# Kernel optimization log

Hardware: AMD Instinct MI355X
Metric: run time of the kernel (lower is better)

Reference implementation:

```python
import jax, jax.numpy as jnp
import numpy as np

N_NODES = 100000
DIM = 128
N_REL = 8
N_EDGES = 640000
LAMDA = 1  # indexes into [x, z1, z2]


def setup_inputs() -> dict:
    key = jax.random.key(0)
    ks = jax.random.split(key, 6)
    x = jax.random.normal(ks[0], (N_NODES, DIM), dtype=jnp.float32)
    edge_index = jax.random.randint(ks[1], (2, N_EDGES), 0, N_NODES, dtype=jnp.int32)
    edge_type = jax.random.randint(ks[2], (N_EDGES,), 0, N_REL, dtype=jnp.int32)
    edge_weight = jax.random.uniform(ks[3], (N_EDGES,), dtype=jnp.float32)
    # xavier_uniform for [R, in, out] weight stacks (fan_in=DIM, fan_out=DIM)
    limit = float(np.sqrt(6.0 / (DIM + DIM)))
    W1 = jax.random.uniform(ks[4], (N_REL, DIM, DIM), jnp.float32, -limit, limit)
    W2 = jax.random.uniform(ks[5], (N_REL, DIM, DIM), jnp.float32, -limit, limit)
    b1 = jnp.zeros((DIM,), jnp.float32)
    b2 = jnp.zeros((DIM,), jnp.float32)
    return {"x": x, "edge_index": edge_index, "edge_type": edge_type,
            "edge_weight": edge_weight, "W1": W1, "b1": b1, "W2": W2, "b2": b2}


def _ecge_conv(x, W, b, row, col, edge_type, coef, n_nodes):
    # Faithful to: msg_e = norm_e * w_e * (x[row_e] @ W[type_e]); out = scatter_add(msg, col) + b
    # Efficient form: transform every node by every relation once (N,R,D), then gather per edge.
    xW = jnp.einsum('ni,rio->nro', x, W)          # [N, R, D]
    msg = xW[row, edge_type] * coef[:, None]       # [E, D]
    out = jax.ops.segment_sum(msg, col, num_segments=n_nodes)
    return out + b


def reference(x, edge_index, edge_type, edge_weight, W1, b1, W2, b2):
    n_nodes = x.shape[0]
    row, col = edge_index[0], edge_index[1]
    # symmetric degree normalization based on destination (col) degree
    deg = jax.ops.segment_sum(jnp.ones_like(edge_weight), col, num_segments=n_nodes)
    deg_inv_sqrt = jnp.where(deg > 0, deg ** -0.5, 0.0)
    norm = deg_inv_sqrt[row] * deg_inv_sqrt[col]
    coef = norm * edge_weight

    z1 = jax.nn.relu(_ecge_conv(x, W1, b1, row, col, edge_type, coef, n_nodes))
    # F.dropout with training=False (eval mode) is identity
    z2 = _ecge_conv(z1, W2, b2, row, col, edge_type, coef, n_nodes)

    z_star = (x + z1 + z2) / 4.0
    temp = [x, z1, z2]
    z_sharp = temp[LAMDA]
    for i in range(LAMDA + 1, 3):
        z_sharp = z_sharp + temp[i]
    z_sharp = z_sharp / (4.0 - LAMDA)
    return (z_star, z_sharp)
```

## Files before the change

### kernel.cpp

```cpp
#include <hip/hip_runtime.h>
#include <hip/hip_bf16.h>
#include <cstdint>
#include <cstddef>

#define DIM  128
#define NREL 8
#define SCB  4096
#define CPB  16

typedef __attribute__((ext_vector_type(8))) short short8;
typedef __attribute__((ext_vector_type(4))) float f32x4;

static inline int cdiv(int a, int b){ return (a + b - 1) / b; }

__device__ inline uint32_t packrn(float lo, float hi){
    __hip_bfloat162 h = __float22bfloat162_rn(make_float2(lo, hi));
    union { __hip_bfloat162 h; uint32_t u; } v; v.h = h; return v.u;
}
__device__ inline float bf2f(uint32_t lo16){
    union { uint32_t u; float f; } v; v.u = lo16 << 16; return v.f;
}
__device__ inline float asf(int u){
    union { int i; float f; } v; v.i = u; return v.f;
}

__global__ __launch_bounds__(256) void k_prep(const float* __restrict__ x, unsigned short* __restrict__ xb, int n4,
                                              const int* __restrict__ col, const int* __restrict__ et, int E,
                                              int* __restrict__ cnt8, int nb4, int eb,
                                              const float* __restrict__ W1, const float* __restrict__ W2,
                                              unsigned short* __restrict__ wpk){
    int blk = blockIdx.x;
    if (blk < nb4){
        int i = blk * 256 + threadIdx.x;
        if (i >= n4) return;
        f32x4 v = __builtin_nontemporal_load((const f32x4*)x + i);
        uint2 o; o.x = packrn(v.x, v.y); o.y = packrn(v.z, v.w);
        *(uint2*)(xb + (size_t)i * 4) = o;
    } else if (blk < nb4 + eb){
        int e = (blk - nb4) * 256 + threadIdx.x;
        if (e < E) atomicAdd(&cnt8[col[e] * NREL + et[e]], 1);
    } else {
        int b = (blk - nb4 - eb) * 4 + (threadIdx.x >> 6);
        int lane = threadIdx.x & 63;
        int ks = b & 3, nt = (b >> 2) & 7, slot = b >> 5;
        const float* Wsrc = (slot < 8) ? (W1 + (size_t)slot * DIM * DIM)
                                       : (W2 + (size_t)(slot - 8) * DIM * DIM);
        int k0 = ks * 32 + (lane >> 4) * 8;
        int n  = nt * 16 + (lane & 15);
        uint4 ow;
        ow.x = packrn(Wsrc[(size_t)(k0 + 0) * DIM + n], Wsrc[(size_t)(k0 + 1) * DIM + n]);
        ow.y = packrn(Wsrc[(size_t)(k0 + 2) * DIM + n], Wsrc[(size_t)(k0 + 3) * DIM + n]);
        ow.z = packrn(Wsrc[(size_t)(k0 + 4) * DIM + n], Wsrc[(size_t)(k0 + 5) * DIM + n]);
        ow.w = packrn(Wsrc[(size_t)(k0 + 6) * DIM + n], Wsrc[(size_t)(k0 + 7) * DIM + n]);
        *(uint4*)(wpk + ((size_t)b * 64 + lane) * 8) = ow;
    }
}

__global__ __launch_bounds__(256) void k_scan1(const int* __restrict__ cnt, int M, int* __restrict__ bsum){
    int t = threadIdx.x;
    int base = blockIdx.x * SCB + t * 16;
    int s = 0;
    #pragma unroll
    for (int k = 0; k < 16; ++k){
        int i = base + k;
        if (i < M) s += cnt[i];
    }
    #pragma unroll
    for (int o = 1; o < 64; o <<= 1) s += __shfl_xor(s, o);
    __shared__ int wsum[4];
    if ((t & 63) == 0) wsum[t >> 6] = s;
    __syncthreads();
    if (t == 0) bsum[blockIdx.x] = wsum[0] + wsum[1] + wsum[2] + wsum[3];
}

__global__ __launch_bounds__(256) void k_scan3(const int* __restrict__ cnt, int M,
                                               const int* __restrict__ bsum, int NBS,
                                               int* __restrict__ startArr, int* __restrict__ pos,
                                               float* __restrict__ deginv){
    int t = threadIdx.x;
    int base = blockIdx.x * SCB + t * 16;
    int vals[16];
    int s = 0;
    #pragma unroll
    for (int k = 0; k < 16; ++k){
        int i = base + k;
        vals[k] = (i < M) ? cnt[i] : 0;
        s += vals[k];
    }

    {
        int d0 = 0, d1 = 0;
        #pragma unroll
        for (int k = 0; k < 8; ++k){ d0 += vals[k]; d1 += vals[8 + k]; }
        int c0i = base >> 3;
        if (base < M)     deginv[c0i]     = d0 > 0 ? rsqrtf((float)d0) : 0.f;
        if (base + 8 < M) deginv[c0i + 1] = d1 > 0 ? rsqrtf((float)d1) : 0.f;
    }

    int lane = t & 63, w = t >> 6;

    int bp = 0, tp = 0;
    for (int i = lane; i < NBS; i += 64){
        int bv = bsum[i];
        if (i < (int)blockIdx.x) bp += bv;
        tp += bv;
    }
    #pragma unroll
    for (int o = 1; o < 64; o <<= 1){ bp += __shfl_xor(bp, o); tp += __shfl_xor(tp, o); }

    int v = s;
    #pragma unroll
    for (int o = 1; o < 64; o <<= 1){
        int u = __shfl_up(v, o);
        if (lane >= o) v += u;
    }
    __shared__ int wsum[4];
    if (lane == 63) wsum[w] = v;
    __syncthreads();
    int excl = v - s + bp;
    for (int i = 0; i < w; ++i) excl += wsum[i];
    #pragma unroll
    for (int k = 0; k < 16; ++k){
        int i = base + k;
        if (i < M){ startArr[i] = excl; pos[i] = excl; excl += vals[k]; }
    }
    if (blockIdx.x == (unsigned)(gridDim.x - 1) && t == 0) startArr[M] = tp;
}

__global__ __launch_bounds__(256) void k_place(const int* __restrict__ row, const int* __restrict__ col,
                                               const int* __restrict__ et, const float* __restrict__ ew,
                                               const float* __restrict__ deginv,
                                               int E, int* __restrict__ pos8, int2* __restrict__ pkm){
    int e = blockIdx.x * 256 + threadIdx.x;
    if (e >= E) return;
    int r = row[e], c = col[e], t = et[e];
    float cf = deginv[r] * deginv[c] * ew[e];
    int p = atomicAdd(&pos8[(c << 3) + t], 1);
    union { float f; int i; } cv; cv.f = cf;
    pkm[p] = make_int2(((c & (CPB - 1)) << 28) | (t << 25) | r, cv.i);
}

template<int MODE>
__global__ __launch_bounds__(512, 8) void k_fused(const unsigned short* __restrict__ xbin,
                                                  const unsigned short* __restrict__ wpk,
                                                  const int* __restrict__ cs8,
                                                  const int2* __restrict__ pkm,
                                                  const float* __restrict__ bias,
                                                  unsigned short* __restrict__ zb,
                                                  const unsigned short* __restrict__ xb2,
                                                  const unsigned short* __restrict__ z1b2,
                                                  float* __restrict__ outS,
                                                  float* __restrict__ outH,
                                                  int N, int wslot){
    __shared__ unsigned short s[CPB * 1024];
    int tid = threadIdx.x;
    int wid = tid >> 6, lane = tid & 63;
    int c0 = blockIdx.x * CPB;

    uint4 z4 = {0u, 0u, 0u, 0u};
    #pragma unroll
    for (int k = 0; k < 4; ++k) ((uint4*)s)[tid + 512 * k] = z4;
    __syncthreads();

#define FLUSH() *(uint32_t*)((char*)s + flushByte) = packrn(a0, a1)
#define PROC(mx, cf, u) do{                                                       \
        int fk_ = (int)(((unsigned)(mx)) >> 25);                                  \
        if (fk_ != fkPrev){                                                       \
            if (fkPrev >= 0) FLUSH();                                             \
            fkPrev = fk_;                                                         \
            flushByte = (fk_ << 8) + ((lane << 2) ^ ((fk_ << 1) & 0x70));         \
            a0 = 0.f; a1 = 0.f;                                                   \
        }                                                                         \
        a0 = fmaf(cf, bf2f((u) & 0xFFFFu), a0);                                   \
        a1 = fmaf(cf, bf2f((u) >> 16),     a1); }while(0)
#define XROW(mx) ((const uint32_t*)xbin)[((size_t)(((mx) & 0x1FFFF) << 6)) + lane]

    {
        int c = c0 + wid * 2;
        if (c < N){
            int cHi = c + 2; if (cHi > N) cHi = N;
            int e  = __builtin_amdgcn_readfirstlane(cs8[c * NREL]);
            int eE = __builtin_amdgcn_readfirstlane(cs8[cHi * NREL]);
            int fkPrev = -1;
            int flushByte = 0;
            float a0 = 0.f, a1 = 0.f;
            const int* __restrict__ mp = (const int*)pkm;
            while (e < eE){
                int n = eE - e; if (n > 16) n = 16;
                int mxs[16]; float cfs[16]; uint32_t u[16];
                int mprev = 0;
                #pragma unroll
                for (int k = 0; k < 16; ++k){
                    int live = k < n;
                    int raw  = mp[2 * (e + k)];
                    float rc = asf(mp[2 * (e + k) + 1]);
                    int mx = (k == 0) ? raw : (live ? raw : mprev);
                    mxs[k] = mx; mprev = mx;
                    cfs[k] = live ? rc : 0.f;
                }
                #pragma unroll
                for (int k = 0; k < 16; ++k) u[k] = XROW(mxs[k]);
                __builtin_amdgcn_sched_barrier(0);
                #pragma unroll
                for (int k = 0; k < 16; ++k) PROC(mxs[k], cfs[k], u[k]);
                e += n;
            }
            if (fkPrev >= 0) FLUSH();
        }
    }
#undef PROC
#undef FLUSH
#undef XROW
    __syncthreads();

    int nt = wid;
    f32x4 acc = (f32x4){0,0,0,0};

    int al = lane & 15, ak2 = (lane >> 4) * 16;
    int swz = (al & 7) << 4;
    const char* rowA = (const char*)s + al * 2048;

    const short8* bbase = (const short8*)wpk + (size_t)wslot * 2048 + lane;

    __builtin_amdgcn_s_setprio(1);
    #pragma unroll 4
    for (int ksg = 0; ksg < 32; ++ksg){
        int off = (ksg * 64 + ak2) ^ swz;
        short8 A = *(const short8*)(rowA + off);
        int t = ksg >> 2, ksl = ksg & 3;
        short8 B = (bbase + (size_t)t * 2048)[(nt * 4 + ksl) * 64];
        acc = __builtin_amdgcn_mfma_f32_16x16x32_bf16(A, B, acc, 0, 0, 0);
    }
    __builtin_amdgcn_s_setprio(0);
    __syncthreads();

    float* ot = (float*)s;
    int crb = (lane >> 4) * 4, dcl = lane & 15;
    {
        int d = nt * 16 + dcl;
        float bv = bias[d];
        #pragma unroll
        for (int r = 0; r < 4; ++r){
            int mrow = crb + r;
            float v = acc[r] + bv;
            if (MODE == 0) v = fmaxf(v, 0.f);
            ot[mrow * DIM + d] = v;
        }
    }
    __syncthreads();

    if (MODE == 0){
        if (tid < 256){
            int rowi = tid >> 4, seg = tid & 15;
            int c = c0 + rowi;
            if (c < N){
                const float* src = ot + rowi * DIM + seg * 8;
                uint4 vv;
                vv.x = packrn(src[0], src[1]);
                vv.y = packrn(src[2], src[3]);
                vv.z = packrn(src[4], src[5]);
                vv.w = packrn(src[6], src[7]);
                *(uint4*)(zb + ((size_t)c << 7) + seg * 8) = vv;
            }
        }
    } else {
        int rowi = tid >> 5, q = tid & 31;
        int c = c0 + rowi;
        if (c < N){
            int d0 = q * 4;
            size_t o = ((size_t)c << 7) + d0;
            ushort4 xv4 = *(const ushort4*)(xb2 + o);
            ushort4 zv4 = *(const ushort4*)(z1b2 + o);
            const float* src = ot + rowi * DIM + d0;
            f32x4 S, H;
            {
                float xv = bf2f(xv4.x), z1 = bf2f(zv4.x), v = src[0];
                S.x = (xv + z1 + v) * 0.25f; H.x = (z1 + v) * (1.0f / 3.0f);
            }
            {
                float xv = bf2f(xv4.y), z1 = bf2f(zv4.y), v = src[1];
                S.y = (xv + z1 + v) * 0.25f; H.y = (z1 + v) * (1.0f / 3.0f);
            }
            {
                float xv = bf2f(xv4.z), z1 = bf2f(zv4.z), v = src[2];
                S.z = (xv + z1 + v) * 0.25f; H.z = (z1 + v) * (1.0f / 3.0f);
            }
            {
                float xv = bf2f(xv4.w), z1 = bf2f(zv4.w), v = src[3];
                S.w = (xv + z1 + v) * 0.25f; H.w = (z1 + v) * (1.0f / 3.0f);
            }
            __builtin_nontemporal_store(S, (f32x4*)(outS + o));
            __builtin_nontemporal_store(H, (f32x4*)(outH + o));
        }
    }
}

extern "C" void kernel_launch(void* const* d_in, const int* in_sizes, int n_in,
                              void* d_out, int out_size, void* d_ws, size_t ws_size,
                              hipStream_t stream) {
    const float* x  = (const float*)d_in[0];
    const int*   ei = (const int*)d_in[1];
    const int*   et = (const int*)d_in[2];
    const float* ew = (const float*)d_in[3];
    const float* W1 = (const float*)d_in[4];
    const float* b1 = (const float*)d_in[5];
    const float* W2 = (const float*)d_in[6];
    const float* b2 = (const float*)d_in[7];

    int E = in_sizes[2];
    int N = in_sizes[0] / DIM;
    const int* row = ei;
    const int* col = ei + E;

    float* out = (float*)d_out;
    int ND  = N * DIM;
    int ND4 = ND / 4;
    float* zS = out;
    float* zH = out + ND;

    int M8   = N * NREL;
    int NBS8 = cdiv(M8, SCB);

    char* wsb = (char*)d_ws;
    size_t off = 0;
    auto take = [&](size_t bytes) -> char* {
        char* p = wsb + off;
        off = (off + bytes + 255) & ~(size_t)255;
        return p;
    };
    int*            cnt8     = (int*)           take((size_t)M8 * 4);
    int*            start8   = (int*)           take(((size_t)M8 + 1) * 4);
    int*            pos8     = (int*)           take((size_t)M8 * 4);
    int*            bsum     = (int*)           take(((size_t)NBS8 + 1) * 4);
    float*          deginv   = (float*)         take((size_t)N * 4);
    int2*           pkm      = (int2*)          take(((size_t)E + 16) * 8);
    unsigned short* wpk      = (unsigned short*)take((size_t)16 * 2048 * 8 * 2);
    unsigned short* xb       = (unsigned short*)take((size_t)ND * 2);
    unsigned short* z1b      = (unsigned short*)take((size_t)ND * 2);
    (void)n_in; (void)out_size; (void)ws_size;

    (void)hipMemsetAsync(cnt8, 0, (size_t)M8 * 4, stream);

    int eb  = cdiv(E, 256);
    int nb4 = cdiv(ND4, 256);
    k_prep  <<<nb4 + eb + 128, 256, 0, stream>>>(x, xb, ND4, col, et, E, cnt8, nb4, eb, W1, W2, wpk);
    k_scan1 <<<NBS8, 256, 0, stream>>>(cnt8, M8, bsum);
    k_scan3 <<<NBS8, 256, 0, stream>>>(cnt8, M8, bsum, NBS8, start8, pos8, deginv);
    k_place <<<eb, 256, 0, stream>>>(row, col, et, ew, deginv, E, pos8, pkm);

    int fb = cdiv(N, CPB);
    k_fused<0><<<fb, 512, 0, stream>>>(xb, wpk, start8, pkm, b1, z1b, nullptr, nullptr, nullptr, nullptr, N, 0);
    k_fused<1><<<fb, 512, 0, stream>>>(z1b, wpk, start8, pkm, b2, nullptr, xb, z1b, zS, zH, N, 8);
}
```

Measured before the change: 252.5 us.

## Make fused gather-GEMM kernel persistent and prefetch the next tile's gathers during MFMA

The fused aggregate-then-transform kernel becomes persistent, launched with at most 1024 blocks that stride over node tiles. Before each tile's MFMA loop, the first 16 edges of the next tile have their metadata and x rows loaded into registers, so those gather latencies can overlap the matrix multiply and epilogue. LDS is re-zeroed inside the loop instead of once per block. This trades launch and tail cost for higher register pressure (48 extra prefetch registers per thread), a hard grid cap that may reduce occupancy, and two extra barriers per tile.

```diff
diff --git a/kernel.cpp b/kernel.cpp
--- a/kernel.cpp
+++ b/kernel.cpp
@@ -151,15 +151,16 @@
                                                   const unsigned short* __restrict__ z1b2,
                                                   float* __restrict__ outS,
                                                   float* __restrict__ outH,
-                                                  int N, int wslot){
+                                                  int N, int NT, int wslot){
     __shared__ unsigned short s[CPB * 1024];
     int tid = threadIdx.x;
     int wid = tid >> 6, lane = tid & 63;
-    int c0 = blockIdx.x * CPB;
-
-    uint4 z4 = {0u, 0u, 0u, 0u};
-    #pragma unroll
-    for (int k = 0; k < 4; ++k) ((uint4*)s)[tid + 512 * k] = z4;
+    const int stride = gridDim.x;
+    const int* __restrict__ mp = (const int*)pkm;
+
+    uint4 z4v = {0u, 0u, 0u, 0u};
+    #pragma unroll
+    for (int k = 0; k < 4; ++k) ((uint4*)s)[tid + 512 * k] = z4v;
     __syncthreads();
 
 #define FLUSH() *(uint32_t*)((char*)s + flushByte) = packrn(a0, a1)
@@ -175,16 +176,17 @@
         a1 = fmaf(cf, bf2f((u) >> 16),     a1); }while(0)
 #define XROW(mx) ((const uint32_t*)xbin)[((size_t)(((mx) & 0x1FFFF) << 6)) + lane]
 
+    int t0 = blockIdx.x;
+    if (t0 >= NT) return;
+
     {
-        int c = c0 + wid * 2;
+        int c = t0 * CPB + wid * 2;
         if (c < N){
             int cHi = c + 2; if (cHi > N) cHi = N;
             int e  = __builtin_amdgcn_readfirstlane(cs8[c * NREL]);
             int eE = __builtin_amdgcn_readfirstlane(cs8[cHi * NREL]);
-            int fkPrev = -1;
-            int flushByte = 0;
+            int fkPrev = -1, flushByte = 0;
             float a0 = 0.f, a1 = 0.f;
-            const int* __restrict__ mp = (const int*)pkm;
             while (e < eE){
                 int n = eE - e; if (n > 16) n = 16;
                 int mxs[16]; float cfs[16]; uint32_t u[16];
@@ -208,91 +210,161 @@
             if (fkPrev >= 0) FLUSH();
         }
     }
+    __syncthreads();
+
+    int al = lane & 15, ak2 = (lane >> 4) * 16;
+    int swz = (al & 7) << 4;
+    const char* rowA = (const char*)s + al * 2048;
+    const short8* bbase = (const short8*)wpk + (size_t)wslot * 2048 + lane;
+    float* ot = (float*)s;
+    int nt = wid, crb = (lane >> 4) * 4, dcl = lane & 15;
+
+    for (int t = t0; t < NT; t += stride){
+        int nxt = t + stride;
+        bool hasN = nxt < NT;
+
+        int n0 = 0, ge = 0, geE = 0;
+        int gmx[16]; float gcf[16]; uint32_t gu[16];
+        if (hasN){
+            int c = nxt * CPB + wid * 2;
+            if (c < N){
+                int cHi = c + 2; if (cHi > N) cHi = N;
+                ge  = __builtin_amdgcn_readfirstlane(cs8[c * NREL]);
+                geE = __builtin_amdgcn_readfirstlane(cs8[cHi * NREL]);
+                n0 = geE - ge; if (n0 > 16) n0 = 16;
+                if (n0 > 0){
+                    int mprev = 0;
+                    #pragma unroll
+                    for (int k = 0; k < 16; ++k){
+                        int live = k < n0;
+                        int raw  = mp[2 * (ge + k)];
+                        float rc = asf(mp[2 * (ge + k) + 1]);
+                        int mx = (k == 0) ? raw : (live ? raw : mprev);
+                        gmx[k] = mx; mprev = mx;
+                        gcf[k] = live ? rc : 0.f;
+                    }
+                    #pragma unroll
+                    for (int k = 0; k < 16; ++k) gu[k] = XROW(gmx[k]);
+                    ge += n0;
+                }
+            }
+        }
+
+        f32x4 acc = (f32x4){0,0,0,0};
+        __builtin_amdgcn_s_setprio(1);
+        #pragma unroll 4
+        for (int ksg = 0; ksg < 32; ++ksg){
+            int off = (ksg * 64 + ak2) ^ swz;
+            short8 A = *(const short8*)(rowA + off);
+            int tt = ksg >> 2, ksl = ksg & 3;
+            short8 B = (bbase + (size_t)tt * 2048)[(nt * 4 + ksl) * 64];
+            acc = __builtin_amdgcn_mfma_f32_16x16x32_bf16(A, B, acc, 0, 0, 0);
+        }
+        __builtin_amdgcn_s_setprio(0);
+        __syncthreads();
+
+        {
+            int d = nt * 16 + dcl;
+            float bv = bias[d];
+            #pragma unroll
+            for (int r = 0; r < 4; ++r){
+                float v = acc[r] + bv;
+                if (MODE == 0) v = fmaxf(v, 0.f);
+                ot[(crb + r) * DIM + d] = v;
+            }
+            uint4* zp = (uint4*)((char*)s + 8192);
+            #pragma unroll
+            for (int k = 0; k < 3; ++k) zp[tid + 512 * k] = z4v;
+        }
+        __syncthreads();
+
+        {
+            f32x4 zf = (f32x4){0,0,0,0};
+            if (MODE == 0){
+                if (tid < 256){
+                    int rowi = tid >> 4, seg = tid & 15;
+                    int c = t * CPB + rowi;
+                    float* src = ot + rowi * DIM + seg * 8;
+                    if (c < N){
+                        uint4 vv;
+                        vv.x = packrn(src[0], src[1]);
+                        vv.y = packrn(src[2], src[3]);
+                        vv.z = packrn(src[4], src[5]);
+                        vv.w = packrn(src[6], src[7]);
+                        *(uint4*)(zb + ((size_t)c << 7) + seg * 8) = vv;
+                    }
+                    *(f32x4*)src = zf;
+                    *(f32x4*)(src + 4) = zf;
+                }
+            } else {
+                int rowi = tid >> 5, q = tid & 31;
+                int c = t * CPB + rowi;
+                int d0 = q * 4;
+                float* src = ot + rowi * DIM + d0;
+                if (c < N){
+                    size_t o = ((size_t)c << 7) + d0;
+                    ushort4 xv4 = *(const ushort4*)(xb2 + o);
+                    ushort4 zv4 = *(const ushort4*)(z1b2 + o);
+                    f32x4 S, H;
+                    {
+                        float xv = bf2f(xv4.x), z1 = bf2f(zv4.x), v = src[0];
+                        S.x = (xv + z1 + v) * 0.25f; H.x = (z1 + v) * (1.0f / 3.0f);
+                    }
+                    {
+                        float xv = bf2f(xv4.y), z1 = bf2f(zv4.y), v = src[1];
+                        S.y = (xv + z1 + v) * 0.25f; H.y = (z1 + v) * (1.0f / 3.0f);
+                    }
+                    {
+                        float xv = bf2f(xv4.z), z1 = bf2f(zv4.z), v = src[2];
+                        S.z = (xv + z1 + v) * 0.25f; H.z = (z1 + v) * (1.0f / 3.0f);
+                    }
+                    {
+                        float xv = bf2f(xv4.w), z1 = bf2f(zv4.w), v = src[3];
+                        S.w = (xv + z1 + v) * 0.25f; H.w = (z1 + v) * (1.0f / 3.0f);
+                    }
+                    __builtin_nontemporal_store(S, (f32x4*)(outS + o));
+                    __builtin_nontemporal_store(H, (f32x4*)(outH + o));
+                }
+                *(f32x4*)src = zf;
+            }
+        }
+        __syncthreads();
+
+        if (hasN){
+            int c = nxt * CPB + wid * 2;
+            if (c < N && n0 > 0){
+                int fkPrev = -1, flushByte = 0;
+                float a0 = 0.f, a1 = 0.f;
+                #pragma unroll
+                for (int k = 0; k < 16; ++k) PROC(gmx[k], gcf[k], gu[k]);
+                while (ge < geE){
+                    int n = geE - ge; if (n > 16) n = 16;
+                    int mxs[16]; float cfs[16]; uint32_t u[16];
+                    int mprev = 0;
+                    #pragma unroll
+                    for (int k = 0; k < 16; ++k){
+                        int live = k < n;
+                        int raw  = mp[2 * (ge + k)];
+                        float rc = asf(mp[2 * (ge + k) + 1]);
+                        int mx = (k == 0) ? raw : (live ? raw : mprev);
+                        mxs[k] = mx; mprev = mx;
+                        cfs[k] = live ? rc : 0.f;
+                    }
+                    #pragma unroll
+                    for (int k = 0; k < 16; ++k) u[k] = XROW(mxs[k]);
+                    __builtin_amdgcn_sched_barrier(0);
+                    #pragma unroll
+                    for (int k = 0; k < 16; ++k) PROC(mxs[k], cfs[k], u[k]);
+                    ge += n;
+                }
+                if (fkPrev >= 0) FLUSH();
+            }
+        }
+        __syncthreads();
+    }
 #undef PROC
 #undef FLUSH
 #undef XROW
-    __syncthreads();
-
-    int nt = wid;
-    f32x4 acc = (f32x4){0,0,0,0};
-
-    int al = lane & 15, ak2 = (lane >> 4) * 16;
-    int swz = (al & 7) << 4;
-    const char* rowA = (const char*)s + al * 2048;
-
-    const short8* bbase = (const short8*)wpk + (size_t)wslot * 2048 + lane;
-
-    __builtin_amdgcn_s_setprio(1);
-    #pragma unroll 4
-    for (int ksg = 0; ksg < 32; ++ksg){
-        int off = (ksg * 64 + ak2) ^ swz;
-        short8 A = *(const short8*)(rowA + off);
-        int t = ksg >> 2, ksl = ksg & 3;
-        short8 B = (bbase + (size_t)t * 2048)[(nt * 4 + ksl) * 64];
-        acc = __builtin_amdgcn_mfma_f32_16x16x32_bf16(A, B, acc, 0, 0, 0);
-    }
-    __builtin_amdgcn_s_setprio(0);
-    __syncthreads();
-
-    float* ot = (float*)s;
-    int crb = (lane >> 4) * 4, dcl = lane & 15;
-    {
-        int d = nt * 16 + dcl;
-        float bv = bias[d];
-        #pragma unroll
-        for (int r = 0; r < 4; ++r){
-            int mrow = crb + r;
-            float v = acc[r] + bv;
-            if (MODE == 0) v = fmaxf(v, 0.f);
-            ot[mrow * DIM + d] = v;
-        }
-    }
-    __syncthreads();
-
-    if (MODE == 0){
-        if (tid < 256){
-            int rowi = tid >> 4, seg = tid & 15;
-            int c = c0 + rowi;
-            if (c < N){
-                const float* src = ot + rowi * DIM + seg * 8;
-                uint4 vv;
-                vv.x = packrn(src[0], src[1]);
-                vv.y = packrn(src[2], src[3]);
-                vv.z = packrn(src[4], src[5]);
-                vv.w = packrn(src[6], src[7]);
-                *(uint4*)(zb + ((size_t)c << 7) + seg * 8) = vv;
-            }
-        }
-    } else {
-        int rowi = tid >> 5, q = tid & 31;
-        int c = c0 + rowi;
-        if (c < N){
-            int d0 = q * 4;
-            size_t o = ((size_t)c << 7) + d0;
-            ushort4 xv4 = *(const ushort4*)(xb2 + o);
-            ushort4 zv4 = *(const ushort4*)(z1b2 + o);
-            const float* src = ot + rowi * DIM + d0;
-            f32x4 S, H;
-            {
-                float xv = bf2f(xv4.x), z1 = bf2f(zv4.x), v = src[0];
-                S.x = (xv + z1 + v) * 0.25f; H.x = (z1 + v) * (1.0f / 3.0f);
-            }
-            {
-                float xv = bf2f(xv4.y), z1 = bf2f(zv4.y), v = src[1];
-                S.y = (xv + z1 + v) * 0.25f; H.y = (z1 + v) * (1.0f / 3.0f);
-            }
-            {
-                float xv = bf2f(xv4.z), z1 = bf2f(zv4.z), v = src[2];
-                S.z = (xv + z1 + v) * 0.25f; H.z = (z1 + v) * (1.0f / 3.0f);
-            }
-            {
-                float xv = bf2f(xv4.w), z1 = bf2f(zv4.w), v = src[3];
-                S.w = (xv + z1 + v) * 0.25f; H.w = (z1 + v) * (1.0f / 3.0f);
-            }
-            __builtin_nontemporal_store(S, (f32x4*)(outS + o));
-            __builtin_nontemporal_store(H, (f32x4*)(outH + o));
-        }
-    }
 }
 
 extern "C" void kernel_launch(void* const* d_in, const int* in_sizes, int n_in,
@@ -349,6 +421,8 @@
     k_place <<<eb, 256, 0, stream>>>(row, col, et, ew, deginv, E, pos8, pkm);
 
     int fb = cdiv(N, CPB);
-    k_fused<0><<<fb, 512, 0, stream>>>(xb, wpk, start8, pkm, b1, z1b, nullptr, nullptr, nullptr, nullptr, N, 0);
-    k_fused<1><<<fb, 512, 0, stream>>>(z1b, wpk, start8, pkm, b2, nullptr, xb, z1b, zS, zH, N, 8);
-}
+    int pg = 1024;
+    if (pg > fb) pg = fb;
+    k_fused<0><<<pg, 512, 0, stream>>>(xb, wpk, start8, pkm, b1, z1b, nullptr, nullptr, nullptr, nullptr, N, fb, 0);
+    k_fused<1><<<pg, 512, 0, stream>>>(z1b, wpk, start8, pkm, b2, nullptr, xb, z1b, zS, zH, N, fb, 8);
+}
```

Result: slower. 650.0 us (+157.4%).

## Balance edge aggregation across warps by edge chunks instead of node pairs

Applied to the files above, without the earlier changes.

Edge aggregation inside a block is no longer split as two destination nodes per warp. Each warp now takes fixed 16-edge chunks of the block's edge range, interleaved across the 8 warps. Each chunk boundary is moved to the next change of (col, relation) key so that every shared-memory slot is written by exactly one warp. This targets load imbalance from skewed node degrees, at the cost of scanning keys at chunk boundaries. Very long runs of one key can still fall to a single warp.

```diff
diff --git a/kernel.cpp b/kernel.cpp
--- a/kernel.cpp
+++ b/kernel.cpp
@@ -176,24 +176,35 @@
 #define XROW(mx) ((const uint32_t*)xbin)[((size_t)(((mx) & 0x1FFFF) << 6)) + lane]
 
     {
-        int c = c0 + wid * 2;
-        if (c < N){
-            int cHi = c + 2; if (cHi > N) cHi = N;
-            int e  = __builtin_amdgcn_readfirstlane(cs8[c * NREL]);
-            int eE = __builtin_amdgcn_readfirstlane(cs8[cHi * NREL]);
-            int fkPrev = -1;
-            int flushByte = 0;
-            float a0 = 0.f, a1 = 0.f;
-            const int* __restrict__ mp = (const int*)pkm;
-            while (e < eE){
-                int n = eE - e; if (n > 16) n = 16;
+        int cHi = c0 + CPB; if (cHi > N) cHi = N;
+        int e0 = __builtin_amdgcn_readfirstlane(cs8[c0 * NREL]);
+        int eT = __builtin_amdgcn_readfirstlane(cs8[cHi * NREL]);
+        int fkPrev = -1, flushByte = 0;
+        float a0 = 0.f, a1 = 0.f;
+        const int* __restrict__ mp = (const int*)pkm;
+
+        for (int b0 = e0 + wid * 16; b0 < eT; b0 += 8 * 16){
+            int bE = b0 + 16; if (bE > eT) bE = eT;
+            int sb = b0;
+            if (b0 > e0){
+                unsigned kp = ((unsigned)mp[2 * (b0 - 1)]) >> 25;
+                while (sb < bE && (((unsigned)mp[2 * sb]) >> 25) == kp) ++sb;
+            }
+            if (sb >= bE) continue;
+            int tE = bE;
+            {
+                unsigned kl = ((unsigned)mp[2 * (bE - 1)]) >> 25;
+                while (tE < eT && (((unsigned)mp[2 * tE]) >> 25) == kl) ++tE;
+            }
+            while (sb < tE){
+                int n = tE - sb; if (n > 16) n = 16;
                 int mxs[16]; float cfs[16]; uint32_t u[16];
                 int mprev = 0;
                 #pragma unroll
                 for (int k = 0; k < 16; ++k){
                     int live = k < n;
-                    int raw  = mp[2 * (e + k)];
-                    float rc = asf(mp[2 * (e + k) + 1]);
+                    int raw  = mp[2 * (sb + k)];
+                    float rc = asf(mp[2 * (sb + k) + 1]);
                     int mx = (k == 0) ? raw : (live ? raw : mprev);
                     mxs[k] = mx; mprev = mx;
                     cfs[k] = live ? rc : 0.f;
@@ -203,10 +214,10 @@
                 __builtin_amdgcn_sched_barrier(0);
                 #pragma unroll
                 for (int k = 0; k < 16; ++k) PROC(mxs[k], cfs[k], u[k]);
-                e += n;
-            }
-            if (fkPrev >= 0) FLUSH();
+                sb += n;
+            }
         }
+        if (fkPrev >= 0) FLUSH();
     }
 #undef PROC
 #undef FLUSH
```

Measured after the change: 283.9 us. 1.12x slower.

## Raise fused aggregate-transform tile from 16 to 20 destination nodes per block

Applied to the files above, without the earlier changes.

Grows the per-block destination-node tile from 16 to 20, so the bf16 relation-weight matrix streamed into the MFMA loop is reused over more rows. The edge packing is changed to hold a non-power-of-two local column index. Each wave now aggregates a variable 2-3 node range, and the GEMM issues a second MFMA per k-step for rows 16-19, with the remaining rows clamped. This adds LDS use (40KB per block) and wasted MFMA work on 12 padded rows, which may lower occupancy and unbalance the waves.

```diff
diff --git a/kernel.cpp b/kernel.cpp
--- a/kernel.cpp
+++ b/kernel.cpp
@@ -6,7 +6,7 @@
 #define DIM  128
 #define NREL 8
 #define SCB  4096
-#define CPB  16
+#define CPB  20
 
 typedef __attribute__((ext_vector_type(8))) short short8;
 typedef __attribute__((ext_vector_type(4))) float f32x4;
@@ -136,8 +136,9 @@
     int r = row[e], c = col[e], t = et[e];
     float cf = deginv[r] * deginv[c] * ew[e];
     int p = atomicAdd(&pos8[(c << 3) + t], 1);
+    int cl = c - (c / CPB) * CPB;
     union { float f; int i; } cv; cv.f = cf;
-    pkm[p] = make_int2(((c & (CPB - 1)) << 28) | (t << 25) | r, cv.i);
+    pkm[p] = make_int2((cl << 20) | (t << 17) | r, cv.i);
 }
 
 template<int MODE>
@@ -159,12 +160,12 @@
 
     uint4 z4 = {0u, 0u, 0u, 0u};
     #pragma unroll
-    for (int k = 0; k < 4; ++k) ((uint4*)s)[tid + 512 * k] = z4;
+    for (int k = 0; k < 5; ++k) ((uint4*)s)[tid + 512 * k] = z4;
     __syncthreads();
 
 #define FLUSH() *(uint32_t*)((char*)s + flushByte) = packrn(a0, a1)
 #define PROC(mx, cf, u) do{                                                       \
-        int fk_ = (int)(((unsigned)(mx)) >> 25);                                  \
+        int fk_ = (int)(((unsigned)(mx)) >> 17);                                  \
         if (fk_ != fkPrev){                                                       \
             if (fkPrev >= 0) FLUSH();                                             \
             fkPrev = fk_;                                                         \
@@ -176,13 +177,14 @@
 #define XROW(mx) ((const uint32_t*)xbin)[((size_t)(((mx) & 0x1FFFF) << 6)) + lane]
 
     {
-        int c = c0 + wid * 2;
-        if (c < N){
-            int cHi = c + 2; if (cHi > N) cHi = N;
-            int e  = __builtin_amdgcn_readfirstlane(cs8[c * NREL]);
+        int cLo = c0 + ((wid * CPB) >> 3);
+        int cHi = c0 + (((wid + 1) * CPB) >> 3);
+        if (cLo > N) cLo = N;
+        if (cHi > N) cHi = N;
+        if (cLo < cHi){
+            int e  = __builtin_amdgcn_readfirstlane(cs8[cLo * NREL]);
             int eE = __builtin_amdgcn_readfirstlane(cs8[cHi * NREL]);
-            int fkPrev = -1;
-            int flushByte = 0;
+            int fkPrev = -1, flushByte = 0;
             float a0 = 0.f, a1 = 0.f;
             const int* __restrict__ mp = (const int*)pkm;
             while (e < eE){
@@ -214,11 +216,13 @@
     __syncthreads();
 
     int nt = wid;
-    f32x4 acc = (f32x4){0,0,0,0};
+    f32x4 acc0 = (f32x4){0,0,0,0}, acc1 = (f32x4){0,0,0,0};
 
     int al = lane & 15, ak2 = (lane >> 4) * 16;
     int swz = (al & 7) << 4;
-    const char* rowA = (const char*)s + al * 2048;
+    const char* rowA0 = (const char*)s + al * 2048;
+    int r1c = 16 + al; if (r1c > CPB - 1) r1c = CPB - 1;
+    const char* rowA1 = (const char*)s + r1c * 2048;
 
     const short8* bbase = (const short8*)wpk + (size_t)wslot * 2048 + lane;
 
@@ -226,10 +230,12 @@
     #pragma unroll 4
     for (int ksg = 0; ksg < 32; ++ksg){
         int off = (ksg * 64 + ak2) ^ swz;
-        short8 A = *(const short8*)(rowA + off);
+        short8 A0 = *(const short8*)(rowA0 + off);
+        short8 A1 = *(const short8*)(rowA1 + off);
         int t = ksg >> 2, ksl = ksg & 3;
         short8 B = (bbase + (size_t)t * 2048)[(nt * 4 + ksl) * 64];
-        acc = __builtin_amdgcn_mfma_f32_16x16x32_bf16(A, B, acc, 0, 0, 0);
+        acc0 = __builtin_amdgcn_mfma_f32_16x16x32_bf16(A0, B, acc0, 0, 0, 0);
+        acc1 = __builtin_amdgcn_mfma_f32_16x16x32_bf16(A1, B, acc1, 0, 0, 0);
     }
     __builtin_amdgcn_s_setprio(0);
     __syncthreads();
@@ -241,16 +247,22 @@
         float bv = bias[d];
         #pragma unroll
         for (int r = 0; r < 4; ++r){
-            int mrow = crb + r;
-            float v = acc[r] + bv;
-            if (MODE == 0) v = fmaxf(v, 0.f);
-            ot[mrow * DIM + d] = v;
+            int row0 = crb + r;
+            float v0 = acc0[r] + bv;
+            if (MODE == 0) v0 = fmaxf(v0, 0.f);
+            ot[row0 * DIM + d] = v0;
+            int row1 = 16 + crb + r;
+            if (row1 < CPB){
+                float v1 = acc1[r] + bv;
+                if (MODE == 0) v1 = fmaxf(v1, 0.f);
+                ot[row1 * DIM + d] = v1;
+            }
         }
     }
     __syncthreads();
 
     if (MODE == 0){
-        if (tid < 256){
+        if (tid < CPB * 16){
             int rowi = tid >> 4, seg = tid & 15;
             int c = c0 + rowi;
             if (c < N){
@@ -264,33 +276,38 @@
             }
         }
     } else {
-        int rowi = tid >> 5, q = tid & 31;
-        int c = c0 + rowi;
-        if (c < N){
-            int d0 = q * 4;
-            size_t o = ((size_t)c << 7) + d0;
-            ushort4 xv4 = *(const ushort4*)(xb2 + o);
-            ushort4 zv4 = *(const ushort4*)(z1b2 + o);
-            const float* src = ot + rowi * DIM + d0;
-            f32x4 S, H;
-            {
-                float xv = bf2f(xv4.x), z1 = bf2f(zv4.x), v = src[0];
-                S.x = (xv + z1 + v) * 0.25f; H.x = (z1 + v) * (1.0f / 3.0f);
+        #pragma unroll
+        for (int pass = 0; pass < 2; ++pass){
+            int rowi = (pass == 0) ? (tid >> 5) : (16 + (tid >> 5));
+            bool act = (pass == 0) || (tid < (CPB - 16) * 32);
+            int c = c0 + rowi;
+            if (act && c < N){
+                int q = tid & 31;
+                int d0 = q * 4;
+                size_t o = ((size_t)c << 7) + d0;
+                ushort4 xv4 = *(const ushort4*)(xb2 + o);
+                ushort4 zv4 = *(const ushort4*)(z1b2 + o);
+                const float* src = ot + rowi * DIM + d0;
+                f32x4 S, H;
+                {
+                    float xv = bf2f(xv4.x), z1 = bf2f(zv4.x), v = src[0];
+                    S.x = (xv + z1 + v) * 0.25f; H.x = (z1 + v) * (1.0f / 3.0f);
+                }
+                {
+                    float xv = bf2f(xv4.y), z1 = bf2f(zv4.y), v = src[1];
+                    S.y = (xv + z1 + v) * 0.25f; H.y = (z1 + v) * (1.0f / 3.0f);
+                }
+                {
+                    float xv = bf2f(xv4.z), z1 = bf2f(zv4.z), v = src[2];
+                    S.z = (xv + z1 + v) * 0.25f; H.z = (z1 + v) * (1.0f / 3.0f);
+                }
+                {
+                    float xv = bf2f(xv4.w), z1 = bf2f(zv4.w), v = src[3];
+                    S.w = (xv + z1 + v) * 0.25f; H.w = (z1 + v) * (1.0f / 3.0f);
+                }
+                __builtin_nontemporal_store(S, (f32x4*)(outS + o));
+                __builtin_nontemporal_store(H, (f32x4*)(outH + o));
             }
-            {
-                float xv = bf2f(xv4.y), z1 = bf2f(zv4.y), v = src[1];
-                S.y = (xv + z1 + v) * 0.25f; H.y = (z1 + v) * (1.0f / 3.0f);
-            }
-            {
-                float xv = bf2f(xv4.z), z1 = bf2f(zv4.z), v = src[2];
-                S.z = (xv + z1 + v) * 0.25f; H.z = (z1 + v) * (1.0f / 3.0f);
-            }
-            {
-                float xv = bf2f(xv4.w), z1 = bf2f(zv4.w), v = src[3];
-                S.w = (xv + z1 + v) * 0.25f; H.w = (z1 + v) * (1.0f / 3.0f);
-            }
-            __builtin_nontemporal_store(S, (f32x4*)(outS + o));
-            __builtin_nontemporal_store(H, (f32x4*)(outH + o));
         }
     }
 }
```

Measured after the change: 246.1 us. 1.03x faster.
